# Performance work log

Measured on AMD Instinct MI355X. Metric: run time of the kernel, lower is better.

The kernel has to match this reference:

```python
import jax, jax.numpy as jnp
import numpy as np
from jax import lax

B, H, OUT, STEPS = 256, 512, 9, 325  # 1 initial step + 325 unrolled steps = 326 outputs


def setup_inputs() -> dict:
    key = jax.random.key(0)
    ks = jax.random.split(key, 12)
    s = 0.05
    return {
        "x": jax.random.normal(ks[0], (B, H), jnp.float32),
        "hx0": jax.random.normal(ks[1], (B, H), jnp.float32),
        "cx0": jax.random.normal(ks[2], (B, H), jnp.float32),
        "W_ih": jax.random.normal(ks[3], (4 * H, H), jnp.float32) * s,
        "W_hh": jax.random.normal(ks[4], (4 * H, H), jnp.float32) * s,
        "b_ih": jax.random.normal(ks[5], (4 * H,), jnp.float32) * s,
        "b_hh": jax.random.normal(ks[6], (4 * H,), jnp.float32) * s,
        "W1": jax.random.normal(ks[7], (H, H), jnp.float32) * s,
        "b1": jax.random.normal(ks[8], (H,), jnp.float32) * s,
        "W2": jax.random.normal(ks[9], (OUT, H), jnp.float32) * s,
        "b2": jax.random.normal(ks[10], (OUT,), jnp.float32) * s,
    }


def reference(x, hx0, cx0, W_ih, W_hh, b_ih, b_hh, W1, b1, W2, b2):
    def lstm_cell(inp, h, c):
        # PyTorch LSTMCell gate order: i, f, g, o
        gates = inp @ W_ih.T + b_ih + h @ W_hh.T + b_hh  # [B, 4H]
        i, f, g, o = jnp.split(gates, 4, axis=-1)
        i = jax.nn.sigmoid(i)
        f = jax.nn.sigmoid(f)
        g = jnp.tanh(g)
        o = jax.nn.sigmoid(o)
        c_new = f * c + i * g
        h_new = o * jnp.tanh(c_new)
        return h_new, c_new

    def mlp(h):
        return jax.nn.relu(h @ W1.T + b1) @ W2.T + b2  # [B, 9]

    h, c = lstm_cell(x, hx0, cx0)
    y0 = mlp(h)

    def step(carry, _):
        h, c = carry
        # original: self.cell(hx, (hx, cx)) -- input IS the current hidden state
        h, c = lstm_cell(h, h, c)
        return (h, c), mlp(h)

    _, ys = lax.scan(step, (h, c), None, length=STEPS)  # ys: [325, B, 9]
    out = jnp.concatenate([y0[None], ys], axis=0)  # [326, B, 9]
    return jnp.transpose(out, (1, 0, 2))  # [B, 326, 9]
```

## Files before the change

### kernel.cpp

```cpp
#include <hip/hip_runtime.h>
#include <cstdio>

#define B_   256
#define H_   512
#define G4_  2048
#define T_   326
#define OUT_ 9

typedef __attribute__((ext_vector_type(8))) short s16x8;
typedef __attribute__((ext_vector_type(4))) float f32x4;

__device__ inline unsigned short to_bf16(float f) {
    unsigned int u = __builtin_bit_cast(unsigned int, f);
    unsigned int r = (u + 0x7fffu + ((u >> 16) & 1u)) >> 16;
    return (unsigned short)r;
}

__device__ inline float sigmoidf_(float x) { return 1.0f / (1.0f + __expf(-x)); }

__device__ inline float fast_tanh(float x) {
    x = fminf(fmaxf(x, -15.f), 15.f);
    float e = __expf(2.f * x);
    return (e - 1.f) / (e + 1.f);
}


__global__ void prep_weights(const float* __restrict__ Wih, const float* __restrict__ Whh,
                             const float* __restrict__ bih, const float* __restrict__ bhh,
                             unsigned short* __restrict__ Wc, unsigned short* __restrict__ Wcat,
                             float* __restrict__ bc) {
    int idx = blockIdx.x * 256 + threadIdx.x;
    int n = idx >> 9, k = idx & 511;
    float wi = Wih[idx], wh = Whh[idx];
    Wc[idx] = to_bf16(wi + wh);
    Wcat[(n << 10) + k]       = to_bf16(wi);
    Wcat[(n << 10) + 512 + k] = to_bf16(wh);
    if (k == 0) bc[n] = bih[n] + bhh[n];
}

__global__ void prep_w1(const float* __restrict__ W1, unsigned short* __restrict__ W1b) {
    int idx = blockIdx.x * 256 + threadIdx.x;
    W1b[idx] = to_bf16(W1[idx]);
}

__global__ void prep_w2(const float* __restrict__ W2, unsigned short* __restrict__ W2b) {
    int idx = blockIdx.x * 256 + threadIdx.x;
    int o = idx >> 9, k = idx & 511;
    W2b[idx] = (o < OUT_) ? to_bf16(W2[o * H_ + k]) : (unsigned short)0;
}

__global__ void prep_x(const float* __restrict__ x, const float* __restrict__ hx0,
                       unsigned short* __restrict__ xcat) {
    int idx = blockIdx.x * 256 + threadIdx.x;
    int b = idx >> 9, k = idx & 511;
    xcat[(b << 10) + k]       = to_bf16(x[idx]);
    xcat[(b << 10) + 512 + k] = to_bf16(hx0[idx]);
}

template <int KLEN>
__global__ __launch_bounds__(256) void lstm_step(
    const unsigned short* __restrict__ A,
    const unsigned short* __restrict__ W,
    const float* __restrict__ bc,
    const float* __restrict__ c_in,
    float* __restrict__ c_out,
    unsigned short* __restrict__ h_out) {
    const int lane = threadIdx.x & 63;
    const int wave = threadIdx.x >> 6;
    const int mn = lane & 15, q = lane >> 4;
    const int rt = blockIdx.x & 15;
    const int hb = (blockIdx.x >> 4) * 64 + wave * 16;

    const unsigned short* ap  = A + (size_t)(rt * 16 + mn) * KLEN + q * 8;
    const unsigned short* wp0 = W + (size_t)(0 * H_ + hb + mn) * KLEN + q * 8;
    const unsigned short* wp1 = W + (size_t)(1 * H_ + hb + mn) * KLEN + q * 8;
    const unsigned short* wp2 = W + (size_t)(2 * H_ + hb + mn) * KLEN + q * 8;
    const unsigned short* wp3 = W + (size_t)(3 * H_ + hb + mn) * KLEN + q * 8;

    f32x4 acc0 = {0.f,0.f,0.f,0.f}, acc1 = {0.f,0.f,0.f,0.f};
    f32x4 acc2 = {0.f,0.f,0.f,0.f}, acc3 = {0.f,0.f,0.f,0.f};
#pragma unroll 4
    for (int k0 = 0; k0 < KLEN; k0 += 32) {
        s16x8 a  = *reinterpret_cast<const s16x8*>(ap + k0);
        s16x8 w0 = *reinterpret_cast<const s16x8*>(wp0 + k0);
        s16x8 w1 = *reinterpret_cast<const s16x8*>(wp1 + k0);
        s16x8 w2 = *reinterpret_cast<const s16x8*>(wp2 + k0);
        s16x8 w3 = *reinterpret_cast<const s16x8*>(wp3 + k0);
        acc0 = __builtin_amdgcn_mfma_f32_16x16x32_bf16(a, w0, acc0, 0, 0, 0);
        acc1 = __builtin_amdgcn_mfma_f32_16x16x32_bf16(a, w1, acc1, 0, 0, 0);
        acc2 = __builtin_amdgcn_mfma_f32_16x16x32_bf16(a, w2, acc2, 0, 0, 0);
        acc3 = __builtin_amdgcn_mfma_f32_16x16x32_bf16(a, w3, acc3, 0, 0, 0);
    }

    const int j = hb + mn;
    const float bi = bc[j], bfv = bc[H_ + j], bg = bc[2 * H_ + j], bo = bc[3 * H_ + j];
#pragma unroll
    for (int r = 0; r < 4; ++r) {
        const int row = rt * 16 + q * 4 + r;
        const float iv = sigmoidf_(acc0[r] + bi);
        const float fv = sigmoidf_(acc1[r] + bfv);
        const float gv = fast_tanh(acc2[r] + bg);
        const float ov = sigmoidf_(acc3[r] + bo);
        const float co = c_in[row * H_ + j];
        const float cn = fv * co + iv * gv;
        c_out[row * H_ + j] = cn;
        h_out[row * H_ + j] = to_bf16(ov * fast_tanh(cn));
    }
}

__global__ __launch_bounds__(256) void lstm_persist(
    const unsigned short* __restrict__ Wc,
    const float* __restrict__ bc,
    const float* __restrict__ c0,
    unsigned short* __restrict__ h_hist,
    unsigned int* __restrict__ ctr) {
    constexpr int AS = 520;
    __shared__ unsigned short A_lds[32 * AS];
    __shared__ float gate_lds[4 * 32 * 17];
    const int tid = threadIdx.x;
    const int lane = tid & 63, wave = tid >> 6;
    const int mn = lane & 15, q = lane >> 4;
    const int mt = blockIdx.x & 7;
    const int jb = (blockIdx.x >> 3) * 16;
    unsigned int* ctr_g = ctr + mt * 32;

    s16x8 breg[16];
    {
        const unsigned short* wp = Wc + (size_t)(wave * H_ + jb + mn) * H_ + q * 8;
#pragma unroll
        for (int kk = 0; kk < 16; ++kk) breg[kk] = *reinterpret_cast<const s16x8*>(wp + kk * 32);
    }
    const float bcv = bc[wave * H_ + jb + mn];

    const int crow = tid >> 3, cc0 = (tid & 7) * 2;
    float c_x = c0[(size_t)(mt * 32 + crow) * H_ + jb + cc0];
    float c_y = c0[(size_t)(mt * 32 + crow) * H_ + jb + cc0 + 1];

    for (int t = 1; t < T_; ++t) {
        const unsigned long long* hsrc64 = reinterpret_cast<const unsigned long long*>(
            h_hist + (size_t)(t - 1) * (B_ * H_) + (size_t)mt * 32 * H_);
        unsigned long long vv[16];
#pragma unroll
        for (int p = 0; p < 16; ++p)
            vv[p] = __hip_atomic_load(hsrc64 + p * 256 + tid, __ATOMIC_RELAXED,
                                      __HIP_MEMORY_SCOPE_AGENT);
#pragma unroll
        for (int p = 0; p < 16; ++p) {
            int qi = p * 256 + tid;
            int row = qi >> 7;
            int col = (qi & 127) << 2;
            *reinterpret_cast<unsigned long long*>(&A_lds[row * AS + col]) = vv[p];
        }
        __syncthreads();

        f32x4 acc0 = {0.f,0.f,0.f,0.f}, acc1 = {0.f,0.f,0.f,0.f};
#pragma unroll
        for (int kk = 0; kk < 16; ++kk) {
            s16x8 a0 = *reinterpret_cast<const s16x8*>(&A_lds[mn * AS + kk * 32 + q * 8]);
            s16x8 a1 = *reinterpret_cast<const s16x8*>(&A_lds[(16 + mn) * AS + kk * 32 + q * 8]);
            acc0 = __builtin_amdgcn_mfma_f32_16x16x32_bf16(a0, breg[kk], acc0, 0, 0, 0);
            acc1 = __builtin_amdgcn_mfma_f32_16x16x32_bf16(a1, breg[kk], acc1, 0, 0, 0);
        }

#pragma unroll
        for (int r = 0; r < 4; ++r) {
            float v0 = acc0[r] + bcv, v1 = acc1[r] + bcv;
            if (wave == 2) { v0 = fast_tanh(v0); v1 = fast_tanh(v1); }
            else           { v0 = sigmoidf_(v0); v1 = sigmoidf_(v1); }
            gate_lds[(wave * 32 + (q * 4 + r)) * 17 + mn]      = v0;
            gate_lds[(wave * 32 + (16 + q * 4 + r)) * 17 + mn] = v1;
        }
        __syncthreads();

        {
            float iv0 = gate_lds[(0 * 32 + crow) * 17 + cc0], iv1 = gate_lds[(0 * 32 + crow) * 17 + cc0 + 1];
            float fv0 = gate_lds[(1 * 32 + crow) * 17 + cc0], fv1 = gate_lds[(1 * 32 + crow) * 17 + cc0 + 1];
            float gv0 = gate_lds[(2 * 32 + crow) * 17 + cc0], gv1 = gate_lds[(2 * 32 + crow) * 17 + cc0 + 1];
            float ov0 = gate_lds[(3 * 32 + crow) * 17 + cc0], ov1 = gate_lds[(3 * 32 + crow) * 17 + cc0 + 1];
            c_x = fv0 * c_x + iv0 * gv0;
            c_y = fv1 * c_y + iv1 * gv1;
            unsigned int h0 = to_bf16(ov0 * fast_tanh(c_x));
            unsigned int h1 = to_bf16(ov1 * fast_tanh(c_y));
            unsigned int packed = h0 | (h1 << 16);
            unsigned int* hdst = reinterpret_cast<unsigned int*>(
                h_hist + (size_t)t * (B_ * H_) + (size_t)(mt * 32 + crow) * H_ + jb + cc0);
            __hip_atomic_store(hdst, packed, __ATOMIC_RELAXED, __HIP_MEMORY_SCOPE_AGENT);
        }

        if (t < T_ - 1) {
            __syncthreads();
            asm volatile("" ::: "memory");
            if (tid == 0) {
                __hip_atomic_fetch_add(ctr_g, 1u, __ATOMIC_RELAXED, __HIP_MEMORY_SCOPE_AGENT);
                const unsigned int target = 32u * (unsigned int)t;
                while (__hip_atomic_load(ctr_g, __ATOMIC_RELAXED, __HIP_MEMORY_SCOPE_AGENT) < target) {
                }
            }
            asm volatile("" ::: "memory");
            __syncthreads();
        }
    }
}

__global__ __launch_bounds__(256) void mlp_kernel(
    const unsigned short* __restrict__ h_hist,
    const unsigned short* __restrict__ W1b,
    const float* __restrict__ b1,
    const unsigned short* __restrict__ W2b,
    const float* __restrict__ b2,
    float* __restrict__ out) {
    constexpr int ZS = 520;
    __shared__ unsigned short z_lds[32 * ZS];

    const int lane = threadIdx.x & 63;
    const int wave = threadIdx.x >> 6;
    const int mn = lane & 15, q = lane >> 4;
    const int t = blockIdx.x >> 2, mt = blockIdx.x & 3;

    const unsigned short* Abase = h_hist + ((size_t)t * B_ + mt * 64) * H_;
    const int nb = wave * 128;

    f32x4 zero4 = {0.f,0.f,0.f,0.f};
    f32x4 acc[4][8];
#pragma unroll
    for (int m4 = 0; m4 < 4; ++m4)
#pragma unroll
        for (int nt = 0; nt < 8; ++nt) acc[m4][nt] = zero4;

    for (int k0 = 0; k0 < 512; k0 += 32) {
        s16x8 a[4];
#pragma unroll
        for (int m4 = 0; m4 < 4; ++m4)
            a[m4] = *reinterpret_cast<const s16x8*>(Abase + (size_t)(m4 * 16 + mn) * H_ + k0 + q * 8);
#pragma unroll
        for (int nt = 0; nt < 8; ++nt) {
            s16x8 b = *reinterpret_cast<const s16x8*>(W1b + (size_t)(nb + nt * 16 + mn) * H_ + k0 + q * 8);
#pragma unroll
            for (int m4 = 0; m4 < 4; ++m4)
                acc[m4][nt] = __builtin_amdgcn_mfma_f32_16x16x32_bf16(a[m4], b, acc[m4][nt], 0, 0, 0);
        }
    }

    float b1v[8];
#pragma unroll
    for (int nt = 0; nt < 8; ++nt) b1v[nt] = b1[nb + nt * 16 + mn];

    for (int pass = 0; pass < 2; ++pass) {
        __syncthreads();
#pragma unroll
        for (int m4i = 0; m4i < 2; ++m4i) {
            const int m4 = 2 * pass + m4i;
            const int rl = m4i * 16 + q * 4;
#pragma unroll
            for (int nt = 0; nt < 8; ++nt) {
                const int col = nb + nt * 16 + mn;
#pragma unroll
                for (int r = 0; r < 4; ++r) {
                    float v = acc[m4][nt][r] + b1v[nt];
                    v = v > 0.f ? v : 0.f;
                    z_lds[(rl + r) * ZS + col] = to_bf16(v);
                }
            }
        }
        __syncthreads();
        if (wave < 2) {
            f32x4 yacc = {0.f,0.f,0.f,0.f};
#pragma unroll 4
            for (int k0 = 0; k0 < 512; k0 += 32) {
                s16x8 az = *reinterpret_cast<const s16x8*>(&z_lds[(wave * 16 + mn) * ZS + k0 + q * 8]);
                s16x8 bw = *reinterpret_cast<const s16x8*>(W2b + (size_t)mn * H_ + k0 + q * 8);
                yacc = __builtin_amdgcn_mfma_f32_16x16x32_bf16(az, bw, yacc, 0, 0, 0);
            }
            if (mn < OUT_) {
                const float bias = b2[mn];
#pragma unroll
                for (int r = 0; r < 4; ++r) {
                    const int row_local = pass * 32 + wave * 16 + q * 4 + r;
                    const int b = mt * 64 + row_local;
                    out[(size_t)b * (T_ * OUT_) + t * OUT_ + mn] = yacc[r] + bias;
                }
            }
        }
    }
}

extern "C" void kernel_launch(void* const* d_in, const int* in_sizes, int n_in,
                              void* d_out, int out_size, void* d_ws, size_t ws_size,
                              hipStream_t stream) {
    (void)in_sizes; (void)n_in; (void)out_size;
    const float* x   = (const float*)d_in[0];
    const float* hx0 = (const float*)d_in[1];
    const float* cx0 = (const float*)d_in[2];
    const float* Wih = (const float*)d_in[3];
    const float* Whh = (const float*)d_in[4];
    const float* bih = (const float*)d_in[5];
    const float* bhh = (const float*)d_in[6];
    const float* W1  = (const float*)d_in[7];
    const float* b1  = (const float*)d_in[8];
    const float* W2  = (const float*)d_in[9];
    const float* b2  = (const float*)d_in[10];
    float* out = (float*)d_out;

    char* p = (char*)d_ws;
    size_t off = 0;
    auto alloc = [&](size_t bytes) {
        void* r = p + off;
        off = (off + bytes + 255) & ~(size_t)255;
        return r;
    };
    unsigned short* Wc     = (unsigned short*)alloc((size_t)G4_ * H_ * 2);
    unsigned short* Wcat   = (unsigned short*)alloc((size_t)G4_ * 1024 * 2);
    unsigned short* W1b    = (unsigned short*)alloc((size_t)H_ * H_ * 2);
    unsigned short* W2b    = (unsigned short*)alloc((size_t)16 * H_ * 2);
    float*          bc     = (float*)alloc((size_t)G4_ * 4);
    unsigned short* xcat   = (unsigned short*)alloc((size_t)B_ * 1024 * 2);
    float*          cbuf   = (float*)alloc((size_t)B_ * H_ * 4);
    unsigned int*   ctr    = (unsigned int*)alloc(4096);
    unsigned short* h_hist = (unsigned short*)alloc((size_t)T_ * B_ * H_ * 2);
    if (off > ws_size) {
        fprintf(stderr, "kernel_launch: ws too small: need %zu have %zu\n", off, ws_size);
        return;
    }

    prep_weights<<<G4_ * H_ / 256, 256, 0, stream>>>(Wih, Whh, bih, bhh, Wc, Wcat, bc);
    prep_w1<<<H_ * H_ / 256, 256, 0, stream>>>(W1, W1b);
    prep_w2<<<16 * H_ / 256, 256, 0, stream>>>(W2, W2b);
    prep_x<<<B_ * H_ / 256, 256, 0, stream>>>(x, hx0, xcat);

    lstm_step<1024><<<128, 256, 0, stream>>>(xcat, Wcat, bc, cx0, cbuf, h_hist);

    hipMemsetAsync(ctr, 0, 4096, stream);
    {
        const unsigned short* Wc_l = Wc;
        const float* bc_l = bc;
        const float* c0_l = cbuf;
        unsigned short* hh_l = h_hist;
        unsigned int* ctr_l = ctr;
        void* args[5] = {(void*)&Wc_l, (void*)&bc_l, (void*)&c0_l, (void*)&hh_l, (void*)&ctr_l};
        hipLaunchCooperativeKernel((const void*)lstm_persist, dim3(256), dim3(256), args, 0, stream);
    }

    mlp_kernel<<<T_ * 4, 256, 0, stream>>>(h_hist, W1b, b1, W2b, b2, out);
}
```

Baseline: 1.200 ms.

## Replace per-group counter barrier with per-block step flags and chunked waits

After: 1.808 ms. 50.7% more time.

```diff
diff --git a/kernel.cpp b/kernel.cpp
--- a/kernel.cpp
+++ b/kernel.cpp
@@ -113,7 +113,7 @@
     const float* __restrict__ bc,
     const float* __restrict__ c0,
     unsigned short* __restrict__ h_hist,
-    unsigned int* __restrict__ ctr) {
+    unsigned int* __restrict__ flg) {
     constexpr int AS = 520;
     __shared__ unsigned short A_lds[32 * AS];
     __shared__ float gate_lds[4 * 32 * 17];
@@ -121,8 +121,9 @@
     const int lane = tid & 63, wave = tid >> 6;
     const int mn = lane & 15, q = lane >> 4;
     const int mt = blockIdx.x & 7;
-    const int jb = (blockIdx.x >> 3) * 16;
-    unsigned int* ctr_g = ctr + mt * 32;
+    const int p  = blockIdx.x >> 3;
+    const int jb = p * 16;
+    unsigned int* my_flag = flg + (mt * 4 + (p >> 3)) * 32 + (p & 7);
 
     s16x8 breg[16];
     {
@@ -136,21 +137,42 @@
     float c_x = c0[(size_t)(mt * 32 + crow) * H_ + jb + cc0];
     float c_y = c0[(size_t)(mt * 32 + crow) * H_ + jb + cc0 + 1];
 
+    const int arow = tid >> 3;
+    const int aw   = (tid & 7) * 4;
+
     for (int t = 1; t < T_; ++t) {
         const unsigned long long* hsrc64 = reinterpret_cast<const unsigned long long*>(
             h_hist + (size_t)(t - 1) * (B_ * H_) + (size_t)mt * 32 * H_);
+        const unsigned int tgt = (unsigned int)(t - 1);
         unsigned long long vv[16];
 #pragma unroll
-        for (int p = 0; p < 16; ++p)
-            vv[p] = __hip_atomic_load(hsrc64 + p * 256 + tid, __ATOMIC_RELAXED,
-                                      __HIP_MEMORY_SCOPE_AGENT);
-#pragma unroll
-        for (int p = 0; p < 16; ++p) {
-            int qi = p * 256 + tid;
-            int row = qi >> 7;
-            int col = (qi & 127) << 2;
-            *reinterpret_cast<unsigned long long*>(&A_lds[row * AS + col]) = vv[p];
-        }
+        for (int kb = 0; kb < 4; ++kb) {
+            const unsigned long long* f64 = reinterpret_cast<const unsigned long long*>(
+                flg + (mt * 4 + kb) * 32);
+            for (;;) {
+                unsigned long long f0 = __hip_atomic_load(f64 + 0, __ATOMIC_RELAXED, __HIP_MEMORY_SCOPE_AGENT);
+                unsigned long long f1 = __hip_atomic_load(f64 + 1, __ATOMIC_RELAXED, __HIP_MEMORY_SCOPE_AGENT);
+                unsigned long long f2 = __hip_atomic_load(f64 + 2, __ATOMIC_RELAXED, __HIP_MEMORY_SCOPE_AGENT);
+                unsigned long long f3 = __hip_atomic_load(f64 + 3, __ATOMIC_RELAXED, __HIP_MEMORY_SCOPE_AGENT);
+                unsigned int m0 = min((unsigned int)f0, (unsigned int)(f0 >> 32));
+                unsigned int m1 = min((unsigned int)f1, (unsigned int)(f1 >> 32));
+                unsigned int m2 = min((unsigned int)f2, (unsigned int)(f2 >> 32));
+                unsigned int m3 = min((unsigned int)f3, (unsigned int)(f3 >> 32));
+                if (min(min(m0, m1), min(m2, m3)) >= tgt) break;
+            }
+            asm volatile("" ::: "memory");
+            const unsigned long long* src = hsrc64 + (size_t)arow * 128 + kb * 32 + aw;
+#pragma unroll
+            for (int j = 0; j < 4; ++j)
+                vv[kb * 4 + j] = __hip_atomic_load(src + j, __ATOMIC_RELAXED,
+                                                   __HIP_MEMORY_SCOPE_AGENT);
+        }
+#pragma unroll
+        for (int kb = 0; kb < 4; ++kb)
+#pragma unroll
+            for (int j = 0; j < 4; ++j)
+                *reinterpret_cast<unsigned long long*>(
+                    &A_lds[arow * AS + (kb * 32 + aw + j) * 4]) = vv[kb * 4 + j];
         __syncthreads();
 
         f32x4 acc0 = {0.f,0.f,0.f,0.f}, acc1 = {0.f,0.f,0.f,0.f};
@@ -190,14 +212,9 @@
         if (t < T_ - 1) {
             __syncthreads();
             asm volatile("" ::: "memory");
-            if (tid == 0) {
-                __hip_atomic_fetch_add(ctr_g, 1u, __ATOMIC_RELAXED, __HIP_MEMORY_SCOPE_AGENT);
-                const unsigned int target = 32u * (unsigned int)t;
-                while (__hip_atomic_load(ctr_g, __ATOMIC_RELAXED, __HIP_MEMORY_SCOPE_AGENT) < target) {
-                }
-            }
-            asm volatile("" ::: "memory");
-            __syncthreads();
+            if (tid == 0)
+                __hip_atomic_store(my_flag, (unsigned int)t, __ATOMIC_RELAXED,
+                                   __HIP_MEMORY_SCOPE_AGENT);
         }
     }
 }
@@ -315,7 +332,7 @@
     float*          bc     = (float*)alloc((size_t)G4_ * 4);
     unsigned short* xcat   = (unsigned short*)alloc((size_t)B_ * 1024 * 2);
     float*          cbuf   = (float*)alloc((size_t)B_ * H_ * 4);
-    unsigned int*   ctr    = (unsigned int*)alloc(4096);
+    unsigned int*   flg    = (unsigned int*)alloc(4096);
     unsigned short* h_hist = (unsigned short*)alloc((size_t)T_ * B_ * H_ * 2);
     if (off > ws_size) {
         fprintf(stderr, "kernel_launch: ws too small: need %zu have %zu\n", off, ws_size);
@@ -329,14 +346,14 @@
 
     lstm_step<1024><<<128, 256, 0, stream>>>(xcat, Wcat, bc, cx0, cbuf, h_hist);
 
-    hipMemsetAsync(ctr, 0, 4096, stream);
+    hipMemsetAsync(flg, 0, 4096, stream);
     {
         const unsigned short* Wc_l = Wc;
         const float* bc_l = bc;
         const float* c0_l = cbuf;
         unsigned short* hh_l = h_hist;
-        unsigned int* ctr_l = ctr;
-        void* args[5] = {(void*)&Wc_l, (void*)&bc_l, (void*)&c0_l, (void*)&hh_l, (void*)&ctr_l};
+        unsigned int* flg_l = flg;
+        void* args[5] = {(void*)&Wc_l, (void*)&bc_l, (void*)&c0_l, (void*)&hh_l, (void*)&flg_l};
         hipLaunchCooperativeKernel((const void*)lstm_persist, dim3(256), dim3(256), args, 0, stream);
     }
 
```

## Retile persistent LSTM blocks to 16 rows x 32 cols with swizzled LDS

Applied to the files above, without the earlier changes.

Result: faster. 1.019 ms (-15.1%).

```diff
diff --git a/kernel.cpp b/kernel.cpp
--- a/kernel.cpp
+++ b/kernel.cpp
@@ -114,76 +114,88 @@
     const float* __restrict__ c0,
     unsigned short* __restrict__ h_hist,
     unsigned int* __restrict__ ctr) {
-    constexpr int AS = 520;
-    __shared__ unsigned short A_lds[32 * AS];
-    __shared__ float gate_lds[4 * 32 * 17];
+    __shared__ unsigned short A_lds[16 * 512];
+    __shared__ float gate_lds[4 * 16 * 33];
     const int tid = threadIdx.x;
     const int lane = tid & 63, wave = tid >> 6;
     const int mn = lane & 15, q = lane >> 4;
-    const int mt = blockIdx.x & 7;
-    const int jb = (blockIdx.x >> 3) * 16;
-    unsigned int* ctr_g = ctr + mt * 32;
-
-    s16x8 breg[16];
-    {
-        const unsigned short* wp = Wc + (size_t)(wave * H_ + jb + mn) * H_ + q * 8;
-#pragma unroll
-        for (int kk = 0; kk < 16; ++kk) breg[kk] = *reinterpret_cast<const s16x8*>(wp + kk * 32);
-    }
-    const float bcv = bc[wave * H_ + jb + mn];
-
-    const int crow = tid >> 3, cc0 = (tid & 7) * 2;
-    float c_x = c0[(size_t)(mt * 32 + crow) * H_ + jb + cc0];
-    float c_y = c0[(size_t)(mt * 32 + crow) * H_ + jb + cc0 + 1];
+    const int g  = blockIdx.x & 15;
+    const int jb = (blockIdx.x >> 4) * 32;
+    unsigned int* ctr_g = ctr + g * 32;
+
+    s16x8 breg[2][16];
+#pragma unroll
+    for (int n = 0; n < 2; ++n) {
+        const unsigned short* wp = Wc + (size_t)(wave * H_ + jb + n * 16 + mn) * H_ + q * 8;
+#pragma unroll
+        for (int kk = 0; kk < 16; ++kk)
+            breg[n][kk] = *reinterpret_cast<const s16x8*>(wp + kk * 32);
+    }
+    const float bcv0 = bc[wave * H_ + jb + mn];
+    const float bcv1 = bc[wave * H_ + jb + 16 + mn];
+
+    const int crow = tid >> 4, cc0 = (tid & 15) * 2;
+    float c_x = c0[(size_t)(g * 16 + crow) * H_ + jb + cc0];
+    float c_y = c0[(size_t)(g * 16 + crow) * H_ + jb + cc0 + 1];
+
+    int a_st[8];
+#pragma unroll
+    for (int p = 0; p < 8; ++p) {
+        const int qi = p * 256 + tid;
+        const int row = qi >> 7;
+        const int bcol = (qi & 127) * 8;
+        a_st[p] = row * 512 + (((bcol) ^ ((row & 7) << 4)) >> 1);
+    }
+    int a_rd[16];
+#pragma unroll
+    for (int kk = 0; kk < 16; ++kk) {
+        const int bcol = kk * 64 + q * 16;
+        a_rd[kk] = mn * 512 + ((bcol ^ ((mn & 7) << 4)) >> 1);
+    }
 
     for (int t = 1; t < T_; ++t) {
         const unsigned long long* hsrc64 = reinterpret_cast<const unsigned long long*>(
-            h_hist + (size_t)(t - 1) * (B_ * H_) + (size_t)mt * 32 * H_);
-        unsigned long long vv[16];
-#pragma unroll
-        for (int p = 0; p < 16; ++p)
+            h_hist + (size_t)(t - 1) * (B_ * H_) + (size_t)g * 16 * H_);
+        unsigned long long vv[8];
+#pragma unroll
+        for (int p = 0; p < 8; ++p)
             vv[p] = __hip_atomic_load(hsrc64 + p * 256 + tid, __ATOMIC_RELAXED,
                                       __HIP_MEMORY_SCOPE_AGENT);
 #pragma unroll
-        for (int p = 0; p < 16; ++p) {
-            int qi = p * 256 + tid;
-            int row = qi >> 7;
-            int col = (qi & 127) << 2;
-            *reinterpret_cast<unsigned long long*>(&A_lds[row * AS + col]) = vv[p];
-        }
+        for (int p = 0; p < 8; ++p)
+            *reinterpret_cast<unsigned long long*>(&A_lds[a_st[p]]) = vv[p];
         __syncthreads();
 
         f32x4 acc0 = {0.f,0.f,0.f,0.f}, acc1 = {0.f,0.f,0.f,0.f};
 #pragma unroll
         for (int kk = 0; kk < 16; ++kk) {
-            s16x8 a0 = *reinterpret_cast<const s16x8*>(&A_lds[mn * AS + kk * 32 + q * 8]);
-            s16x8 a1 = *reinterpret_cast<const s16x8*>(&A_lds[(16 + mn) * AS + kk * 32 + q * 8]);
-            acc0 = __builtin_amdgcn_mfma_f32_16x16x32_bf16(a0, breg[kk], acc0, 0, 0, 0);
-            acc1 = __builtin_amdgcn_mfma_f32_16x16x32_bf16(a1, breg[kk], acc1, 0, 0, 0);
+            s16x8 a = *reinterpret_cast<const s16x8*>(&A_lds[a_rd[kk]]);
+            acc0 = __builtin_amdgcn_mfma_f32_16x16x32_bf16(a, breg[0][kk], acc0, 0, 0, 0);
+            acc1 = __builtin_amdgcn_mfma_f32_16x16x32_bf16(a, breg[1][kk], acc1, 0, 0, 0);
         }
 
 #pragma unroll
         for (int r = 0; r < 4; ++r) {
-            float v0 = acc0[r] + bcv, v1 = acc1[r] + bcv;
+            float v0 = acc0[r] + bcv0, v1 = acc1[r] + bcv1;
             if (wave == 2) { v0 = fast_tanh(v0); v1 = fast_tanh(v1); }
             else           { v0 = sigmoidf_(v0); v1 = sigmoidf_(v1); }
-            gate_lds[(wave * 32 + (q * 4 + r)) * 17 + mn]      = v0;
-            gate_lds[(wave * 32 + (16 + q * 4 + r)) * 17 + mn] = v1;
+            gate_lds[(wave * 16 + (q * 4 + r)) * 33 + mn]      = v0;
+            gate_lds[(wave * 16 + (q * 4 + r)) * 33 + 16 + mn] = v1;
         }
         __syncthreads();
 
         {
-            float iv0 = gate_lds[(0 * 32 + crow) * 17 + cc0], iv1 = gate_lds[(0 * 32 + crow) * 17 + cc0 + 1];
-            float fv0 = gate_lds[(1 * 32 + crow) * 17 + cc0], fv1 = gate_lds[(1 * 32 + crow) * 17 + cc0 + 1];
-            float gv0 = gate_lds[(2 * 32 + crow) * 17 + cc0], gv1 = gate_lds[(2 * 32 + crow) * 17 + cc0 + 1];
-            float ov0 = gate_lds[(3 * 32 + crow) * 17 + cc0], ov1 = gate_lds[(3 * 32 + crow) * 17 + cc0 + 1];
+            float iv0 = gate_lds[(0 * 16 + crow) * 33 + cc0], iv1 = gate_lds[(0 * 16 + crow) * 33 + cc0 + 1];
+            float fv0 = gate_lds[(1 * 16 + crow) * 33 + cc0], fv1 = gate_lds[(1 * 16 + crow) * 33 + cc0 + 1];
+            float gv0 = gate_lds[(2 * 16 + crow) * 33 + cc0], gv1 = gate_lds[(2 * 16 + crow) * 33 + cc0 + 1];
+            float ov0 = gate_lds[(3 * 16 + crow) * 33 + cc0], ov1 = gate_lds[(3 * 16 + crow) * 33 + cc0 + 1];
             c_x = fv0 * c_x + iv0 * gv0;
             c_y = fv1 * c_y + iv1 * gv1;
             unsigned int h0 = to_bf16(ov0 * fast_tanh(c_x));
             unsigned int h1 = to_bf16(ov1 * fast_tanh(c_y));
             unsigned int packed = h0 | (h1 << 16);
             unsigned int* hdst = reinterpret_cast<unsigned int*>(
-                h_hist + (size_t)t * (B_ * H_) + (size_t)(mt * 32 + crow) * H_ + jb + cc0);
+                h_hist + (size_t)t * (B_ * H_) + (size_t)(g * 16 + crow) * H_ + jb + cc0);
             __hip_atomic_store(hdst, packed, __ATOMIC_RELAXED, __HIP_MEMORY_SCOPE_AGENT);
         }
 
@@ -192,7 +204,7 @@
             asm volatile("" ::: "memory");
             if (tid == 0) {
                 __hip_atomic_fetch_add(ctr_g, 1u, __ATOMIC_RELAXED, __HIP_MEMORY_SCOPE_AGENT);
-                const unsigned int target = 32u * (unsigned int)t;
+                const unsigned int target = 16u * (unsigned int)t;
                 while (__hip_atomic_load(ctr_g, __ATOMIC_RELAXED, __HIP_MEMORY_SCOPE_AGENT) < target) {
                 }
             }
```
